# Performance work log

Measured on AMD Instinct MI355X. Metric: run time of the kernel, lower is better.

The kernel has to match this reference:

```python
import jax, jax.numpy as jnp
import numpy as np

INPUT_SIZE = 768
HIDDEN = [512, 256, 128]
LATENT = 32
NUM_LEVELS = 3
CODEBOOK_SIZE = 256
BATCH = 131072


def _init_linear(key, d_in, d_out):
    kw, kb = jax.random.split(key)
    lim = 1.0 / np.sqrt(d_in)
    W = jax.random.uniform(kw, (d_in, d_out), jnp.float32, -lim, lim)
    b = jax.random.uniform(kb, (d_out,), jnp.float32, -lim, lim)
    return W, b


def setup_inputs() -> dict:
    key = jax.random.key(0)
    keys = jax.random.split(key, 16)
    inp = {"x": jax.random.normal(keys[0], (BATCH, INPUT_SIZE), jnp.float32)}
    enc_dims = [INPUT_SIZE] + HIDDEN + [LATENT]          # 768->512->256->128->32
    dec_dims = [LATENT] + HIDDEN[::-1] + [INPUT_SIZE]     # 32->128->256->512->768
    for i in range(4):
        W, b = _init_linear(keys[1 + i], enc_dims[i], enc_dims[i + 1])
        inp[f"enc_W{i}"], inp[f"enc_b{i}"] = W, b
        W, b = _init_linear(keys[6 + i], dec_dims[i], dec_dims[i + 1])
        inp[f"dec_W{i}"], inp[f"dec_b{i}"] = W, b
    inp["codebooks"] = jax.random.normal(keys[12], (NUM_LEVELS, CODEBOOK_SIZE, LATENT), jnp.float32)
    return inp


def _mlp(x, Ws, bs):
    # Linear -> ReLU (-> Dropout p=0, identity) between layers, final layer linear.
    n = len(Ws)
    for i in range(n):
        x = x @ Ws[i] + bs[i]
        if i < n - 1:
            x = jax.nn.relu(x)
    return x


def _quantize(z, codebooks):
    # Residual vector quantization over NUM_LEVELS codebooks.
    L, K, D = codebooks.shape
    r = z
    idxs, rs, es = [], [], []
    for l in range(L):
        c = codebooks[l]                                  # [K, D]
        # squared-distance argmin (same argmin as cdist)
        d = jnp.sum(r * r, axis=-1, keepdims=True) - 2.0 * (r @ c.T) + jnp.sum(c * c, axis=-1)
        idx = jnp.argmin(d, axis=-1)                      # [B]
        e = c[idx]                                        # [B, D] gather
        idxs.append(idx)
        rs.append(r)
        es.append(e)
        r = r - e
    quantized = jnp.stack(idxs, axis=1)                   # [B, L] int codes
    r_stack = jnp.stack(rs, axis=1)                       # [B, L, D] residual inputs per level
    e_stack = jnp.stack(es, axis=1)                       # [B, L, D] selected embeddings
    sum_e = jnp.sum(e_stack, axis=1)                      # [B, D]
    # straight-through estimator
    z_hat = z + jax.lax.stop_gradient(sum_e - z)
    counts = jnp.sum(jax.nn.one_hot(quantized, K, dtype=jnp.float32), axis=0)  # [L, K] usage
    return quantized, r_stack, e_stack, z_hat, counts


def reference(x,
              enc_W0, enc_b0, enc_W1, enc_b1, enc_W2, enc_b2, enc_W3, enc_b3,
              dec_W0, dec_b0, dec_W1, dec_b1, dec_W2, dec_b2, dec_W3, dec_b3,
              codebooks):
    encoded = _mlp(x, [enc_W0, enc_W1, enc_W2, enc_W3], [enc_b0, enc_b1, enc_b2, enc_b3])
    quantized, r, e, z_hat, counts = _quantize(encoded, codebooks)
    decoded = _mlp(z_hat, [dec_W0, dec_W1, dec_W2, dec_W3], [dec_b0, dec_b1, dec_b2, dec_b3])
    return decoded, r, e, counts, quantized
```

## Files before the change

### kernel.cpp

```cpp
#include <hip/hip_runtime.h>
#include <hip/hip_bf16.h>
#include <cfloat>

#define B_TOTAL 131072
#define IN_DIM  768
#define NLEV    3
#define KCODE   256

typedef unsigned short u16;
typedef unsigned int   u32;
typedef __attribute__((ext_vector_type(8))) short bf16x8;
typedef __attribute__((ext_vector_type(4))) float f32x4;

#define GLOAD_LDS(g, l)                                                        \
    __builtin_amdgcn_global_load_lds(                                          \
        (const __attribute__((address_space(1))) u32*)(g),                     \
        (__attribute__((address_space(3))) u32*)(l), 16, 0, 0)

__device__ __forceinline__ u16 f2bf(float x) {
    union { __hip_bfloat16 h; u16 u; } c;
    c.h = __float2bfloat16(x);
    return c.u;
}
__device__ __forceinline__ float bf2f(u32 lo16) {
    union { u32 v; float f; } c;
    c.v = lo16 << 16;
    return c.f;
}
__device__ __forceinline__ u32 pack2(float a, float b) {
    return (u32)f2bf(a) | ((u32)f2bf(b) << 16);
}

template<int K, int N, bool AF32, bool RELU, bool OUTF32>
__global__ __launch_bounds__(256)
void gemm_mfma(const void* __restrict__ A_, const u16* __restrict__ Wt,
               const float* __restrict__ bias, void* __restrict__ C_)
{
    constexpr int NK  = K / 32;
    constexpr int NCB = N / 128;
    __shared__ u16 As[3][4096];
    __shared__ u16 Bs[3][4096];

    const int tid  = threadIdx.x;
    const int lane = tid & 63;
    const int wid  = tid >> 6;
    const int wrow = wid >> 1, wcol = wid & 1;

    const u32 nwg  = gridDim.x;
    const u32 orig = blockIdx.x;
    const u32 xcd = orig & 7u, q8 = nwg >> 3, r8 = nwg & 7u;
    const u32 wg = (xcd < r8 ? xcd * (q8 + 1) : r8 * (q8 + 1) + (xcd - r8) * q8)
                 + (orig >> 3);
    const int col0 = (int)(wg % NCB) * 128;
    const int row0 = (int)(wg / NCB) * 128;

    const u16*   Ab = (const u16*)A_;
    const float* Af = (const float*)A_;

    f32x4 acc[4][4];
    #pragma unroll
    for (int i = 0; i < 4; ++i)
        #pragma unroll
        for (int j = 0; j < 4; ++j) acc[i][j] = (f32x4){0.f, 0.f, 0.f, 0.f};

    auto stage_one = [&](u16* dstbase, const u16* src) {
        #pragma unroll
        for (int i = 0; i < 2; ++i) {
            const u32 o   = (u32)(i * 4096 + wid * 1024 + lane * 16);
            const u32 row = o >> 6;
            const u32 cbs = (o & 63u) ^ ((row & 3u) << 4);
            GLOAD_LDS((const char*)(src + (size_t)row * K) + cbs,
                      dstbase + (i * 2048 + wid * 512));
        }
    };
    auto stage_tile = [&](int buf, int kt) {
        stage_one(&Bs[buf][0], Wt + (size_t)col0 * K + kt * 32);
        stage_one(&As[buf][0], Ab + (size_t)row0 * K + kt * 32);
    };

    auto compute = [&](int buf) {
        const char* Ab8 = (const char*)&As[buf][0];
        const char* Bb8 = (const char*)&Bs[buf][0];
        const int kb = (lane >> 4) * 16;
        bf16x8 af[4], bf[4];
        #pragma unroll
        for (int mf = 0; mf < 4; ++mf) {
            const int r = wrow * 64 + mf * 16 + (lane & 15);
            af[mf] = *(const bf16x8*)(Ab8 + r * 64 + (kb ^ ((r & 3) << 4)));
        }
        #pragma unroll
        for (int nf = 0; nf < 4; ++nf) {
            const int r = wcol * 64 + nf * 16 + (lane & 15);
            bf[nf] = *(const bf16x8*)(Bb8 + r * 64 + (kb ^ ((r & 3) << 4)));
        }
        #pragma unroll
        for (int mf = 0; mf < 4; ++mf)
            #pragma unroll
            for (int nf = 0; nf < 4; ++nf)
                acc[mf][nf] = __builtin_amdgcn_mfma_f32_16x16x32_bf16(
                    af[mf], bf[nf], acc[mf][nf], 0, 0, 0);
    };

    if constexpr (AF32) {
        float4 fa[4];
        auto loadA = [&](int kt) {
            const int row = tid >> 1;
            const int ce0 = (tid & 1) * 16;
            const float* s = &Af[(size_t)(row0 + row) * K + kt * 32 + ce0];
            fa[0] = *(const float4*)(s + 0);
            fa[1] = *(const float4*)(s + 4);
            fa[2] = *(const float4*)(s + 8);
            fa[3] = *(const float4*)(s + 12);
        };
        auto writeA = [&](int buf) {
            const int row = tid >> 1;
            const int cb0 = (tid & 1) * 32;
            const int sw  = (row & 3) << 4;
            char* lb = (char*)&As[buf][0] + row * 64;
            *(uint4*)(lb + ((cb0 + 0) ^ sw)) = make_uint4(
                pack2(fa[0].x, fa[0].y), pack2(fa[0].z, fa[0].w),
                pack2(fa[1].x, fa[1].y), pack2(fa[1].z, fa[1].w));
            *(uint4*)(lb + ((cb0 + 16) ^ sw)) = make_uint4(
                pack2(fa[2].x, fa[2].y), pack2(fa[2].z, fa[2].w),
                pack2(fa[3].x, fa[3].y), pack2(fa[3].z, fa[3].w));
        };
        loadA(0);
        stage_one(&Bs[0][0], Wt + (size_t)col0 * K);
        writeA(0);
        __syncthreads();
        int cur = 0;
        #pragma unroll 1
        for (int kt = 0; kt < NK; ++kt) {
            const bool pref = (kt + 1 < NK);
            if (pref) {
                loadA(kt + 1);
                stage_one(&Bs[cur ^ 1][0], Wt + (size_t)col0 * K + (kt + 1) * 32);
            }
            compute(cur);
            if (pref) writeA(cur ^ 1);
            __syncthreads();
            cur ^= 1;
        }
    } else {
        stage_tile(0, 0);
        if (NK > 1) stage_tile(1, 1);
        int cb_ = 0, sb_ = 2;
        #pragma unroll 1
        for (int kt = 0; kt < NK; ++kt) {
            if (kt == NK - 1) asm volatile("s_waitcnt vmcnt(0)");
            else              asm volatile("s_waitcnt vmcnt(4)");
            __builtin_amdgcn_sched_barrier(0);
            __builtin_amdgcn_s_barrier();
            __builtin_amdgcn_sched_barrier(0);
            if (kt + 2 < NK) stage_tile(sb_, kt + 2);
            compute(cb_);
            cb_ = (cb_ == 2) ? 0 : cb_ + 1;
            sb_ = (sb_ == 2) ? 0 : sb_ + 1;
        }
    }

    #pragma unroll
    for (int nf = 0; nf < 4; ++nf) {
        const int col = col0 + wcol * 64 + nf * 16 + (lane & 15);
        const float bv = bias[col];
        #pragma unroll
        for (int mf = 0; mf < 4; ++mf) {
            const int rbase = row0 + wrow * 64 + mf * 16 + (lane >> 4) * 4;
            #pragma unroll
            for (int r = 0; r < 4; ++r) {
                float o = acc[mf][nf][r] + bv;
                if (RELU) o = fmaxf(o, 0.f);
                if constexpr (OUTF32)
                    ((float*)C_)[(size_t)(rbase + r) * N + col] = o;
                else
                    ((u16*)C_)[(size_t)(rbase + r) * N + col] = f2bf(o);
            }
        }
    }
}

template<int K, int N>
__global__ __launch_bounds__(256)
void wcvt(const float* __restrict__ W, u16* __restrict__ Wt)
{
    const int idx = blockIdx.x * 256 + threadIdx.x;
    const int k = idx / N, n = idx - k * N;
    Wt[(size_t)n * K + k] = f2bf(W[idx]);
}

__global__ __launch_bounds__(256)
void xcvt(const float* __restrict__ x, u16* __restrict__ xb)
{
    const size_t n8 = (size_t)B_TOTAL * IN_DIM / 8;
    const size_t stride = (size_t)gridDim.x * 256;
    for (size_t i = (size_t)blockIdx.x * 256 + threadIdx.x; i < n8; i += stride) {
        const float4 a = *(const float4*)&x[i * 8 + 0];
        const float4 b = *(const float4*)&x[i * 8 + 4];
        *(uint4*)&xb[i * 8] = make_uint4(
            pack2(a.x, a.y), pack2(a.z, a.w),
            pack2(b.x, b.y), pack2(b.z, b.w));
    }
}

__global__ __launch_bounds__(256)
void vq_kernel(const u16* __restrict__ h3, const float* __restrict__ eW3,
               const float* __restrict__ eb3, const float* __restrict__ cb,
               float* __restrict__ r_out, float* __restrict__ e_out,
               float* __restrict__ q_out, u16* __restrict__ se_ws,
               u32* __restrict__ ghist, size_t grow_base)
{
    __shared__ float W3[128 * 32];
    __shared__ float ebv[32];
    __shared__ float clds[256 * 36];
    __shared__ float cc2[256];
    __shared__ u32   lh[NLEV * KCODE];

    const int tid = threadIdx.x;
    const size_t lrow = (size_t)blockIdx.x * 256 + tid;
    const size_t grow = grow_base + lrow;

    for (int i = tid; i < 128 * 32; i += 256) W3[i] = eW3[i];
    if (tid < 32) ebv[tid] = eb3[tid];
    for (int i = tid; i < NLEV * KCODE; i += 256) lh[i] = 0;
    __syncthreads();

    float r[32];
    #pragma unroll
    for (int j = 0; j < 32; ++j) r[j] = ebv[j];
    {
        const u32* hrow = (const u32*)h3 + lrow * 64;
        #pragma unroll 2
        for (int k2 = 0; k2 < 64; ++k2) {
            const u32 v = hrow[k2];
            const float x0 = bf2f(v & 0xffffu), x1 = bf2f(v >> 16);
            const float* w0 = &W3[(2 * k2) * 32];
            const float* w1 = &W3[(2 * k2 + 1) * 32];
            #pragma unroll
            for (int j4 = 0; j4 < 8; ++j4) {
                const float4 a = *(const float4*)&w0[4 * j4];
                const float4 b = *(const float4*)&w1[4 * j4];
                r[4*j4+0] = fmaf(x1, b.x, fmaf(x0, a.x, r[4*j4+0]));
                r[4*j4+1] = fmaf(x1, b.y, fmaf(x0, a.y, r[4*j4+1]));
                r[4*j4+2] = fmaf(x1, b.z, fmaf(x0, a.z, r[4*j4+2]));
                r[4*j4+3] = fmaf(x1, b.w, fmaf(x0, a.w, r[4*j4+3]));
            }
        }
    }

    float z0[32];
    #pragma unroll
    for (int j = 0; j < 32; ++j) z0[j] = r[j];

    #pragma unroll 1
    for (int l = 0; l < NLEV; ++l) {
        __syncthreads();
        {
            const float* cl = cb + ((size_t)l * KCODE + tid) * 32;
            float s = 0.f;
            #pragma unroll
            for (int m = 0; m < 8; ++m) {
                const float4 v = *(const float4*)&cl[4 * m];
                *(float4*)&clds[tid * 36 + 4 * m] = v;
                s = fmaf(v.x, v.x, s); s = fmaf(v.y, v.y, s);
                s = fmaf(v.z, v.z, s); s = fmaf(v.w, v.w, s);
            }
            cc2[tid] = -0.5f * s;
        }
        __syncthreads();

        float best = -FLT_MAX;
        int   bidx = 0;
        #pragma unroll 1
        for (int k = 0; k < KCODE; ++k) {
            const float* ck = &clds[k * 36];
            float d0 = 0.f, d1 = 0.f, d2 = 0.f, d3 = 0.f;
            #pragma unroll
            for (int m = 0; m < 8; m += 4) {
                const float4 v0 = *(const float4*)&ck[4 * (m + 0)];
                const float4 v1 = *(const float4*)&ck[4 * (m + 1)];
                const float4 v2 = *(const float4*)&ck[4 * (m + 2)];
                const float4 v3 = *(const float4*)&ck[4 * (m + 3)];
                d0 = fmaf(r[4*m+0],  v0.x, d0); d0 = fmaf(r[4*m+1],  v0.y, d0);
                d0 = fmaf(r[4*m+2],  v0.z, d0); d0 = fmaf(r[4*m+3],  v0.w, d0);
                d1 = fmaf(r[4*m+4],  v1.x, d1); d1 = fmaf(r[4*m+5],  v1.y, d1);
                d1 = fmaf(r[4*m+6],  v1.z, d1); d1 = fmaf(r[4*m+7],  v1.w, d1);
                d2 = fmaf(r[4*m+8],  v2.x, d2); d2 = fmaf(r[4*m+9],  v2.y, d2);
                d2 = fmaf(r[4*m+10], v2.z, d2); d2 = fmaf(r[4*m+11], v2.w, d2);
                d3 = fmaf(r[4*m+12], v3.x, d3); d3 = fmaf(r[4*m+13], v3.y, d3);
                d3 = fmaf(r[4*m+14], v3.z, d3); d3 = fmaf(r[4*m+15], v3.w, d3);
            }
            const float s = ((d0 + d1) + (d2 + d3)) + cc2[k];
            if (s > best) { best = s; bidx = k; }
        }

        const size_t base = (grow * NLEV + l) * 32;
        const float* ce = &clds[bidx * 36];
        #pragma unroll
        for (int m = 0; m < 8; ++m) {
            const float4 ev = *(const float4*)&ce[4 * m];
            *(float4*)&r_out[base + 4 * m] =
                make_float4(r[4*m+0], r[4*m+1], r[4*m+2], r[4*m+3]);
            *(float4*)&e_out[base + 4 * m] = ev;
            r[4*m+0] -= ev.x; r[4*m+1] -= ev.y;
            r[4*m+2] -= ev.z; r[4*m+3] -= ev.w;
        }
        q_out[grow * NLEV + l] = (float)bidx;
        atomicAdd(&lh[l * KCODE + bidx], 1u);
    }

    u32* sed = (u32*)se_ws + lrow * 16;
    #pragma unroll
    for (int m = 0; m < 16; ++m)
        sed[m] = pack2(z0[2*m] - r[2*m], z0[2*m+1] - r[2*m+1]);

    __syncthreads();
    for (int i = tid; i < NLEV * KCODE; i += 256)
        if (lh[i]) atomicAdd(&ghist[i], lh[i]);
}

__global__ void zero_hist(u32* h) {
    if (threadIdx.x < NLEV * KCODE) h[threadIdx.x] = 0;
}
__global__ void counts_fin(const u32* __restrict__ g, float* __restrict__ o) {
    if (threadIdx.x < NLEV * KCODE) o[threadIdx.x] = (float)g[threadIdx.x];
}

__global__ __launch_bounds__(256)
void counts_k(const float* __restrict__ q, float* __restrict__ cnt)
{
    const int l = blockIdx.x >> 8;
    const int k = blockIdx.x & 255;
    const float pat = (float)k;
    int c = 0;
    for (int i = threadIdx.x; i < B_TOTAL; i += 256)
        c += (q[(size_t)i * NLEV + l] == pat) ? 1 : 0;
    __shared__ int red[256];
    red[threadIdx.x] = c;
    __syncthreads();
    for (int s = 128; s > 0; s >>= 1) {
        if (threadIdx.x < s) red[threadIdx.x] += red[threadIdx.x + s];
        __syncthreads();
    }
    if (threadIdx.x == 0)
        cnt[blockIdx.x] = (float)red[0];
}

template<int K, int N, bool RELU, bool AGLOBAL>
static __device__ __forceinline__
void layer16(const float* __restrict__ A, size_t grow0,
             const float* __restrict__ W, const float* __restrict__ bias,
             float* __restrict__ C)
{
    constexpr int QPT = N / 128;
    const int tr = threadIdx.x >> 5;
    const int tc = threadIdx.x & 31;
    float acc[2][QPT * 4];
    #pragma unroll
    for (int i = 0; i < 2; ++i)
        #pragma unroll
        for (int j = 0; j < QPT * 4; ++j) acc[i][j] = 0.f;
    #pragma unroll 2
    for (int k0 = 0; k0 < K; k0 += 4) {
        float4 av[2];
        #pragma unroll
        for (int i = 0; i < 2; ++i) {
            if (AGLOBAL)
                av[i] = *(const float4*)&A[(grow0 + tr * 2 + i) * (size_t)K + k0];
            else
                av[i] = *(const float4*)&A[(tr * 2 + i) * K + k0];
        }
        #pragma unroll
        for (int kk = 0; kk < 4; ++kk) {
            #pragma unroll
            for (int q = 0; q < QPT; ++q) {
                const float4 w4 = *(const float4*)&W[(size_t)(k0 + kk) * N + 4 * (tc + 32 * q)];
                #pragma unroll
                for (int i = 0; i < 2; ++i) {
                    const float a = ((const float*)&av[i])[kk];
                    acc[i][4*q+0] = fmaf(a, w4.x, acc[i][4*q+0]);
                    acc[i][4*q+1] = fmaf(a, w4.y, acc[i][4*q+1]);
                    acc[i][4*q+2] = fmaf(a, w4.z, acc[i][4*q+2]);
                    acc[i][4*q+3] = fmaf(a, w4.w, acc[i][4*q+3]);
                }
            }
        }
    }
    #pragma unroll
    for (int q = 0; q < QPT; ++q) {
        const float4 b4 = *(const float4*)&bias[4 * (tc + 32 * q)];
        #pragma unroll
        for (int i = 0; i < 2; ++i) {
            float4 o;
            o.x = acc[i][4*q+0] + b4.x; o.y = acc[i][4*q+1] + b4.y;
            o.z = acc[i][4*q+2] + b4.z; o.w = acc[i][4*q+3] + b4.w;
            if (RELU) {
                o.x = fmaxf(o.x, 0.f); o.y = fmaxf(o.y, 0.f);
                o.z = fmaxf(o.z, 0.f); o.w = fmaxf(o.w, 0.f);
            }
            *(float4*)&C[(tr * 2 + i) * N + 4 * (tc + 32 * q)] = o;
        }
    }
}

static __device__ __forceinline__
void layer_final16(const float* __restrict__ A, const float* __restrict__ W,
                   const float* __restrict__ bias, float* __restrict__ Cg, size_t grow0)
{
    constexpr int QPT = 6;
    const int tr = threadIdx.x >> 5;
    const int tc = threadIdx.x & 31;
    float acc[2][QPT * 4];
    #pragma unroll
    for (int i = 0; i < 2; ++i)
        #pragma unroll
        for (int j = 0; j < QPT * 4; ++j) acc[i][j] = 0.f;
    #pragma unroll 2
    for (int k0 = 0; k0 < 512; k0 += 4) {
        float4 av[2];
        #pragma unroll
        for (int i = 0; i < 2; ++i)
            av[i] = *(const float4*)&A[(tr * 2 + i) * 512 + k0];
        #pragma unroll
        for (int kk = 0; kk < 4; ++kk) {
            #pragma unroll
            for (int q = 0; q < QPT; ++q) {
                const float4 w4 = *(const float4*)&W[(size_t)(k0 + kk) * 768 + 4 * (tc + 32 * q)];
                #pragma unroll
                for (int i = 0; i < 2; ++i) {
                    const float a = ((const float*)&av[i])[kk];
                    acc[i][4*q+0] = fmaf(a, w4.x, acc[i][4*q+0]);
                    acc[i][4*q+1] = fmaf(a, w4.y, acc[i][4*q+1]);
                    acc[i][4*q+2] = fmaf(a, w4.z, acc[i][4*q+2]);
                    acc[i][4*q+3] = fmaf(a, w4.w, acc[i][4*q+3]);
                }
            }
        }
    }
    #pragma unroll
    for (int q = 0; q < QPT; ++q) {
        const float4 b4 = *(const float4*)&bias[4 * (tc + 32 * q)];
        #pragma unroll
        for (int i = 0; i < 2; ++i) {
            float4 s;
            s.x = acc[i][4*q+0] + b4.x; s.y = acc[i][4*q+1] + b4.y;
            s.z = acc[i][4*q+2] + b4.z; s.w = acc[i][4*q+3] + b4.w;
            *(float4*)&Cg[(grow0 + tr * 2 + i) * (size_t)768 + 4 * (tc + 32 * q)] = s;
        }
    }
}

static __device__ __forceinline__
void layer_narrow16(const float* __restrict__ A, const float* __restrict__ W,
                    const float* __restrict__ bias, float* __restrict__ Z)
{
    const int row = threadIdx.x >> 4;
    const int g   = threadIdx.x & 15;
    float a0 = 0.f, a1 = 0.f;
    #pragma unroll 4
    for (int k0 = 0; k0 < 128; k0 += 4) {
        const float4 av = *(const float4*)&A[row * 128 + k0];
        #pragma unroll
        for (int kk = 0; kk < 4; ++kk) {
            const float2 w2 = *(const float2*)&W[(k0 + kk) * 32 + 2 * g];
            const float a = ((const float*)&av)[kk];
            a0 = fmaf(a, w2.x, a0);
            a1 = fmaf(a, w2.y, a1);
        }
    }
    Z[row * 36 + 2 * g + 0] = a0 + bias[2 * g + 0];
    Z[row * 36 + 2 * g + 1] = a1 + bias[2 * g + 1];
}

__global__ __launch_bounds__(256)
void enc_vq_kernel(const float* __restrict__ x,
                   const float* __restrict__ eW0, const float* __restrict__ eb0,
                   const float* __restrict__ eW1, const float* __restrict__ eb1,
                   const float* __restrict__ eW2, const float* __restrict__ eb2,
                   const float* __restrict__ eW3, const float* __restrict__ eb3,
                   const float* __restrict__ cb,
                   float* __restrict__ r_out, float* __restrict__ e_out,
                   float* __restrict__ q_out)
{
    __shared__ __align__(16) char smem[59648];
    float* h1   = (float*)(smem);
    float* h2   = (float*)(smem + 32768);
    float* h3   = (float*)(smem + 49152);
    float* z    = (float*)(smem + 57344);
    float* clds = (float*)(smem);
    float* cc   = (float*)(smem + 36864);

    const size_t grow0 = (size_t)blockIdx.x * 16;
    layer16<768, 512, true, true >(x,  grow0, eW0, eb0, h1);
    __syncthreads();
    layer16<512, 256, true, false>(h1, 0,     eW1, eb1, h2);
    __syncthreads();
    layer16<256, 128, true, false>(h2, 0,     eW2, eb2, h3);
    __syncthreads();
    layer_narrow16(h3, eW3, eb3, z);

    const int row = threadIdx.x >> 4;
    const int g   = threadIdx.x & 15;
    const size_t grow = grow0 + row;

    #pragma unroll 1
    for (int l = 0; l < NLEV; ++l) {
        __syncthreads();
        {
            const float* cl = cb + (size_t)l * KCODE * 32;
            const int t = threadIdx.x;
            float s = 0.f;
            #pragma unroll
            for (int m = 0; m < 8; ++m) {
                const float4 v = *(const float4*)&cl[t * 32 + 4 * m];
                *(float4*)&clds[t * 36 + 4 * m] = v;
                s = fmaf(v.x, v.x, s); s = fmaf(v.y, v.y, s);
                s = fmaf(v.z, v.z, s); s = fmaf(v.w, v.w, s);
            }
            cc[t] = s;
        }
        __syncthreads();

        float r[32];
        #pragma unroll
        for (int m = 0; m < 8; ++m) {
            const float4 v = *(const float4*)&z[row * 36 + 4 * m];
            r[4*m+0] = v.x; r[4*m+1] = v.y; r[4*m+2] = v.z; r[4*m+3] = v.w;
        }
        float rr = 0.f;
        #pragma unroll
        for (int j = 0; j < 32; ++j) rr = fmaf(r[j], r[j], rr);

        float best = FLT_MAX;
        int   bidx = 0x7fffffff;
        #pragma unroll 1
        for (int t = 0; t < 16; ++t) {
            const int k = g + 16 * t;
            const float* ck = &clds[k * 36];
            float d0 = 0.f, d1 = 0.f, d2 = 0.f, d3 = 0.f;
            #pragma unroll
            for (int m = 0; m < 8; m += 4) {
                const float4 v0 = *(const float4*)&ck[4 * (m + 0)];
                const float4 v1 = *(const float4*)&ck[4 * (m + 1)];
                const float4 v2 = *(const float4*)&ck[4 * (m + 2)];
                const float4 v3 = *(const float4*)&ck[4 * (m + 3)];
                d0 = fmaf(r[4*m+0],  v0.x, d0); d0 = fmaf(r[4*m+1],  v0.y, d0);
                d0 = fmaf(r[4*m+2],  v0.z, d0); d0 = fmaf(r[4*m+3],  v0.w, d0);
                d1 = fmaf(r[4*m+4],  v1.x, d1); d1 = fmaf(r[4*m+5],  v1.y, d1);
                d1 = fmaf(r[4*m+6],  v1.z, d1); d1 = fmaf(r[4*m+7],  v1.w, d1);
                d2 = fmaf(r[4*m+8],  v2.x, d2); d2 = fmaf(r[4*m+9],  v2.y, d2);
                d2 = fmaf(r[4*m+10], v2.z, d2); d2 = fmaf(r[4*m+11], v2.w, d2);
                d3 = fmaf(r[4*m+12], v3.x, d3); d3 = fmaf(r[4*m+13], v3.y, d3);
                d3 = fmaf(r[4*m+14], v3.z, d3); d3 = fmaf(r[4*m+15], v3.w, d3);
            }
            const float dot = (d0 + d1) + (d2 + d3);
            const float d = (rr - 2.f * dot) + cc[k];
            if (d < best || (d == best && k < bidx)) { best = d; bidx = k; }
        }
        #pragma unroll
        for (int off = 1; off < 16; off <<= 1) {
            const float ob = __shfl_xor(best, off);
            const int   oi = __shfl_xor(bidx, off);
            if (ob < best || (ob == best && oi < bidx)) { best = ob; bidx = oi; }
        }

        const float evx = clds[bidx * 36 + 2 * g + 0];
        const float evy = clds[bidx * 36 + 2 * g + 1];
        *(float2*)&r_out[(grow * NLEV + l) * 32 + 2 * g] = make_float2(r[2*g], r[2*g+1]);
        *(float2*)&e_out[(grow * NLEV + l) * 32 + 2 * g] = make_float2(evx, evy);
        if (g == 0) q_out[grow * NLEV + l] = (float)bidx;
        z[row * 36 + 2 * g + 0] = r[2 * g + 0] - evx;
        z[row * 36 + 2 * g + 1] = r[2 * g + 1] - evy;
    }
}

__global__ __launch_bounds__(256)
void dec_kernel(const float* __restrict__ e_in,
                const float* __restrict__ dW0, const float* __restrict__ db0,
                const float* __restrict__ dW1, const float* __restrict__ db1,
                const float* __restrict__ dW2, const float* __restrict__ db2,
                const float* __restrict__ dW3, const float* __restrict__ db3,
                float* __restrict__ dec_out)
{
    __shared__ __align__(16) char smem[59392];
    float* h3 = (float*)(smem);
    float* h2 = (float*)(smem + 32768);
    float* h1 = (float*)(smem + 49152);
    float* se = (float*)(smem + 57344);

    const size_t grow0 = (size_t)blockIdx.x * 16;
    const int row = threadIdx.x >> 4;
    const int g   = threadIdx.x & 15;
    {
        const size_t base = ((grow0 + row) * NLEV) * 32 + 2 * g;
        float s0 = 0.f, s1 = 0.f;
        #pragma unroll
        for (int l = 0; l < NLEV; ++l) {
            const float2 v = *(const float2*)&e_in[base + l * 32];
            s0 += v.x; s1 += v.y;
        }
        se[row * 32 + 2 * g + 0] = s0;
        se[row * 32 + 2 * g + 1] = s1;
    }
    __syncthreads();
    layer16<32,  128, true, false>(se, 0, dW0, db0, h1);
    __syncthreads();
    layer16<128, 256, true, false>(h1, 0, dW1, db1, h2);
    __syncthreads();
    layer16<256, 512, true, false>(h2, 0, dW2, db2, h3);
    __syncthreads();
    layer_final16(h3, dW3, db3, dec_out, grow0);
}

extern "C" void kernel_launch(void* const* d_in, const int* in_sizes, int n_in,
                              void* d_out, int out_size, void* d_ws, size_t ws_size,
                              hipStream_t stream)
{
    (void)in_sizes; (void)n_in; (void)out_size;
    const float* x  = (const float*)d_in[0];
    const float* cb = (const float*)d_in[17];
    const float *eW[4], *eb[4], *dW[4], *db[4];
    for (int i = 0; i < 4; ++i) {
        eW[i] = (const float*)d_in[1 + 4 * i];
        eb[i] = (const float*)d_in[2 + 4 * i];
        dW[i] = (const float*)d_in[3 + 4 * i];
        db[i] = (const float*)d_in[4 + 4 * i];
    }

    float* out = (float*)d_out;
    const size_t OFF_R = (size_t)B_TOTAL * IN_DIM;
    const size_t OFF_E = OFF_R + (size_t)B_TOTAL * NLEV * 32;
    const size_t OFF_C = OFF_E + (size_t)B_TOTAL * NLEV * 32;
    const size_t OFF_Q = OFF_C + (size_t)NLEV * KCODE;

    const size_t WTB = 2236416;
    const size_t XBB = (size_t)B_TOTAL * IN_DIM * 2;
    size_t R = 0;
    bool usexb = false;
    for (size_t cand = 131072; cand >= 2048; cand >>= 1)
        if (WTB + XBB + cand * 3648 + 4096 <= ws_size) { R = cand; usexb = true; break; }
    if (!R)
        for (size_t cand = 131072; cand >= 2048; cand >>= 1)
            if (WTB + cand * 3648 + 4096 <= ws_size) { R = cand; break; }

    if (R && d_ws) {
        u16* Wp   = (u16*)d_ws;
        u16* WtE0 = Wp;
        u16* WtE1 = WtE0 + 393216;
        u16* WtE2 = WtE1 + 131072;
        u16* WtD0 = WtE2 + 32768;
        u16* WtD1 = WtD0 + 4096;
        u16* WtD2 = WtD1 + 32768;
        u16* WtD3 = WtD2 + 131072;
        u16* Wend = WtD3 + 393216;
        u16* xb   = Wend;
        u16* bufs = usexb ? xb + (size_t)B_TOTAL * IN_DIM : Wend;
        u16* h1   = bufs;
        u16* h2   = h1 + R * 512;
        u16* h3   = h2 + R * 256;
        u16* se   = h3 + R * 128;
        u16* d1   = se + R * 32;
        u16* d2   = d1 + R * 128;
        u16* d3   = d2 + R * 256;
        u32* ghist = (u32*)(d3 + R * 512);

        wcvt<768, 512><<<dim3((768 * 512) / 256), 256, 0, stream>>>(eW[0], WtE0);
        wcvt<512, 256><<<dim3((512 * 256) / 256), 256, 0, stream>>>(eW[1], WtE1);
        wcvt<256, 128><<<dim3((256 * 128) / 256), 256, 0, stream>>>(eW[2], WtE2);
        wcvt<32,  128><<<dim3((32 * 128) / 256),  256, 0, stream>>>(dW[0], WtD0);
        wcvt<128, 256><<<dim3((128 * 256) / 256), 256, 0, stream>>>(dW[1], WtD1);
        wcvt<256, 512><<<dim3((256 * 512) / 256), 256, 0, stream>>>(dW[2], WtD2);
        wcvt<512, 768><<<dim3((512 * 768) / 256), 256, 0, stream>>>(dW[3], WtD3);
        zero_hist<<<1, 768, 0, stream>>>(ghist);
        if (usexb)
            xcvt<<<dim3(4096), 256, 0, stream>>>(x, xb);

        const int nch = B_TOTAL / (int)R;
        const int MB = (int)R / 128;
        for (int c = 0; c < nch; ++c) {
            const size_t rb = (size_t)c * R;
            if (usexb)
                gemm_mfma<768, 512, false, true, false><<<dim3(4 * MB), 256, 0, stream>>>(
                    xb + rb * 768, WtE0, eb[0], h1);
            else
                gemm_mfma<768, 512, true,  true, false><<<dim3(4 * MB), 256, 0, stream>>>(
                    x + rb * 768, WtE0, eb[0], h1);
            gemm_mfma<512, 256, false, true,  false><<<dim3(2 * MB), 256, 0, stream>>>(
                h1, WtE1, eb[1], h2);
            gemm_mfma<256, 128, false, true,  false><<<dim3(1 * MB), 256, 0, stream>>>(
                h2, WtE2, eb[2], h3);
            vq_kernel<<<dim3((int)R / 256), 256, 0, stream>>>(
                h3, eW[3], eb[3], cb,
                out + OFF_R, out + OFF_E, out + OFF_Q, se, ghist, rb);
            gemm_mfma<32,  128, false, true,  false><<<dim3(1 * MB), 256, 0, stream>>>(
                se, WtD0, db[0], d1);
            gemm_mfma<128, 256, false, true,  false><<<dim3(2 * MB), 256, 0, stream>>>(
                d1, WtD1, db[1], d2);
            gemm_mfma<256, 512, false, true,  false><<<dim3(4 * MB), 256, 0, stream>>>(
                d2, WtD2, db[2], d3);
            gemm_mfma<512, 768, false, false, true ><<<dim3(6 * MB), 256, 0, stream>>>(
                d3, WtD3, db[3], out + rb * 768);
        }
        counts_fin<<<1, 768, 0, stream>>>(ghist, out + OFF_C);
    } else {
        enc_vq_kernel<<<dim3(B_TOTAL / 16), 256, 0, stream>>>(
            x, eW[0], eb[0], eW[1], eb[1], eW[2], eb[2], eW[3], eb[3], cb,
            out + OFF_R, out + OFF_E, out + OFF_Q);
        counts_k<<<dim3(NLEV * KCODE), 256, 0, stream>>>(out + OFF_Q, out + OFF_C);
        dec_kernel<<<dim3(B_TOTAL / 16), 256, 0, stream>>>(
            out + OFF_E, dW[0], db[0], dW[1], db[1], dW[2], db[2], dW[3], db[3], out);
    }
}
```

Measured before the change: 891.6 us.

## Fuse fp32 input conversion into first GEMM with triple-buffered pipeline

Drops the separate pass that converts the whole fp32 input to bf16 in workspace. The first encoder GEMM now always reads fp32 directly and converts while staging into shared memory. Its fp32-A path is rebuilt as a three-stage pipeline with explicit vmcnt waits and a raw barrier, so global loads run two tiles ahead. This removes a full extra read/write of the input, but relies on the fp32 GEMM path keeping up, and the manual waitcnt counting must match the number of outstanding loads.

```diff
diff --git a/kernel.cpp b/kernel.cpp
--- a/kernel.cpp
+++ b/kernel.cpp
@@ -124,22 +124,29 @@
                 pack2(fa[2].x, fa[2].y), pack2(fa[2].z, fa[2].w),
                 pack2(fa[3].x, fa[3].y), pack2(fa[3].z, fa[3].w));
         };
+
         loadA(0);
         stage_one(&Bs[0][0], Wt + (size_t)col0 * K);
         writeA(0);
-        __syncthreads();
-        int cur = 0;
+        if (NK > 1) {
+            loadA(1);
+            stage_one(&Bs[1][0], Wt + (size_t)col0 * K + 32);
+        }
+
         #pragma unroll 1
         for (int kt = 0; kt < NK; ++kt) {
-            const bool pref = (kt + 1 < NK);
-            if (pref) {
-                loadA(kt + 1);
-                stage_one(&Bs[cur ^ 1][0], Wt + (size_t)col0 * K + (kt + 1) * 32);
-            }
-            compute(cur);
-            if (pref) writeA(cur ^ 1);
-            __syncthreads();
-            cur ^= 1;
+            if (kt == NK - 1) asm volatile("s_waitcnt vmcnt(0) lgkmcnt(0)");
+            else              asm volatile("s_waitcnt vmcnt(6) lgkmcnt(0)");
+            __builtin_amdgcn_sched_barrier(0);
+            __builtin_amdgcn_s_barrier();
+            __builtin_amdgcn_sched_barrier(0);
+            if (kt + 1 < NK) writeA((kt + 1) % 3);
+            if (kt + 2 < NK) {
+                loadA(kt + 2);
+                stage_one(&Bs[(kt + 2) % 3][0],
+                          Wt + (size_t)col0 * K + (kt + 2) * 32);
+            }
+            compute(kt % 3);
         }
     } else {
         stage_tile(0, 0);
@@ -189,20 +196,6 @@
 }
 
 __global__ __launch_bounds__(256)
-void xcvt(const float* __restrict__ x, u16* __restrict__ xb)
-{
-    const size_t n8 = (size_t)B_TOTAL * IN_DIM / 8;
-    const size_t stride = (size_t)gridDim.x * 256;
-    for (size_t i = (size_t)blockIdx.x * 256 + threadIdx.x; i < n8; i += stride) {
-        const float4 a = *(const float4*)&x[i * 8 + 0];
-        const float4 b = *(const float4*)&x[i * 8 + 4];
-        *(uint4*)&xb[i * 8] = make_uint4(
-            pack2(a.x, a.y), pack2(a.z, a.w),
-            pack2(b.x, b.y), pack2(b.z, b.w));
-    }
-}
-
-__global__ __launch_bounds__(256)
 void vq_kernel(const u16* __restrict__ h3, const float* __restrict__ eW3,
                const float* __restrict__ eb3, const float* __restrict__ cb,
                float* __restrict__ r_out, float* __restrict__ e_out,
@@ -633,14 +626,9 @@
     const size_t OFF_Q = OFF_C + (size_t)NLEV * KCODE;
 
     const size_t WTB = 2236416;
-    const size_t XBB = (size_t)B_TOTAL * IN_DIM * 2;
     size_t R = 0;
-    bool usexb = false;
     for (size_t cand = 131072; cand >= 2048; cand >>= 1)
-        if (WTB + XBB + cand * 3648 + 4096 <= ws_size) { R = cand; usexb = true; break; }
-    if (!R)
-        for (size_t cand = 131072; cand >= 2048; cand >>= 1)
-            if (WTB + cand * 3648 + 4096 <= ws_size) { R = cand; break; }
+        if (WTB + cand * 3648 + 4096 <= ws_size) { R = cand; break; }
 
     if (R && d_ws) {
         u16* Wp   = (u16*)d_ws;
@@ -651,10 +639,7 @@
         u16* WtD1 = WtD0 + 4096;
         u16* WtD2 = WtD1 + 32768;
         u16* WtD3 = WtD2 + 131072;
-        u16* Wend = WtD3 + 393216;
-        u16* xb   = Wend;
-        u16* bufs = usexb ? xb + (size_t)B_TOTAL * IN_DIM : Wend;
-        u16* h1   = bufs;
+        u16* h1   = WtD3 + 393216;
         u16* h2   = h1 + R * 512;
         u16* h3   = h2 + R * 256;
         u16* se   = h3 + R * 128;
@@ -671,19 +656,13 @@
         wcvt<256, 512><<<dim3((256 * 512) / 256), 256, 0, stream>>>(dW[2], WtD2);
         wcvt<512, 768><<<dim3((512 * 768) / 256), 256, 0, stream>>>(dW[3], WtD3);
         zero_hist<<<1, 768, 0, stream>>>(ghist);
-        if (usexb)
-            xcvt<<<dim3(4096), 256, 0, stream>>>(x, xb);
 
         const int nch = B_TOTAL / (int)R;
         const int MB = (int)R / 128;
         for (int c = 0; c < nch; ++c) {
             const size_t rb = (size_t)c * R;
-            if (usexb)
-                gemm_mfma<768, 512, false, true, false><<<dim3(4 * MB), 256, 0, stream>>>(
-                    xb + rb * 768, WtE0, eb[0], h1);
-            else
-                gemm_mfma<768, 512, true,  true, false><<<dim3(4 * MB), 256, 0, stream>>>(
-                    x + rb * 768, WtE0, eb[0], h1);
+            gemm_mfma<768, 512, true,  true,  false><<<dim3(4 * MB), 256, 0, stream>>>(
+                x + rb * 768, WtE0, eb[0], h1);
             gemm_mfma<512, 256, false, true,  false><<<dim3(2 * MB), 256, 0, stream>>>(
                 h1, WtE1, eb[1], h2);
             gemm_mfma<256, 128, false, true,  false><<<dim3(1 * MB), 256, 0, stream>>>(
```

Result: faster. 862.6 us (-3.3%).
